# Optimization experiments

Hardware: AMD Instinct MI355X
Metric: run time of the kernel (lower is better)

## Reference

```python
import jax, jax.numpy as jnp
import numpy as np

HIDDEN = 1024
HEADS = 16
HEAD_DIM = HIDDEN // HEADS


def setup_inputs() -> dict:
    key = jax.random.key(0)
    ks = jax.random.split(key, 9)
    B, S, D = 8, 1370, HIDDEN
    x = jax.random.normal(ks[0], (B, S, D), dtype=jnp.float32)
    s = 1.0 / np.sqrt(D)
    Wq = jax.random.normal(ks[1], (D, D), dtype=jnp.float32) * s
    bq = jnp.zeros((D,), dtype=jnp.float32)
    Wk = jax.random.normal(ks[2], (D, D), dtype=jnp.float32) * s
    bk = jnp.zeros((D,), dtype=jnp.float32)
    Wv = jax.random.normal(ks[3], (D, D), dtype=jnp.float32) * s
    bv = jnp.zeros((D,), dtype=jnp.float32)
    Wo = jax.random.normal(ks[4], (D, D), dtype=jnp.float32) * s
    bo = jnp.zeros((D,), dtype=jnp.float32)
    return {"x": x, "Wq": Wq, "bq": bq, "Wk": Wk, "bk": bk,
            "Wv": Wv, "bv": bv, "Wo": Wo, "bo": bo}


def reference(x, Wq, bq, Wk, bk, Wv, bv, Wo, bo):
    B, S, D = x.shape
    H, Dh = HEADS, HEAD_DIM
    # separate Q/K/V projections
    q = (x @ Wq + bq).reshape(B, S, H, Dh).transpose(0, 2, 1, 3)  # [B,H,S,Dh]
    k = (x @ Wk + bk).reshape(B, S, H, Dh).transpose(0, 2, 1, 3)
    v = (x @ Wv + bv).reshape(B, S, H, Dh).transpose(0, 2, 1, 3)
    scale = jnp.asarray(Dh, q.dtype) ** -0.5
    attn = jnp.einsum('bhqd,bhkd->bhqk', q, k) * scale  # [B,H,S,S]
    attn = jax.nn.softmax(attn, axis=-1)
    out = jnp.einsum('bhqk,bhkd->bhqd', attn, v)        # [B,H,S,Dh]
    out = out.transpose(0, 2, 1, 3).reshape(B, S, D)
    return out @ Wo + bo
```

## Files before the change

kernel.cpp:

```cpp
#include <hip/hip_runtime.h>
#include <stdint.h>

#define DEV __device__ __forceinline__

typedef unsigned short u16;
typedef __attribute__((ext_vector_type(8))) __bf16 bf16x8;
typedef __attribute__((ext_vector_type(8))) u16 u16x8;
typedef __attribute__((ext_vector_type(4))) u16 u16x4;
typedef __attribute__((ext_vector_type(4))) float floatx4;

#define S_LEN 1370
#define S_PAD 1408
#define NH 16
#define DH 64
#define M_TOK (8 * S_LEN)
#define NKT (S_PAD / 64)
#define CEXP 0.18033688f

DEV u16 f2bf(float f) {
    union { float f; uint32_t u; } v; v.f = f;
    uint32_t u = v.u + 0x7fffu + ((v.u >> 16) & 1u);
    return (u16)(u >> 16);
}

typedef const __attribute__((address_space(1))) void as1_cvoid;
typedef __attribute__((address_space(3))) void as3_void;

DEV void async16(const void* g, void* s) {
    __builtin_amdgcn_global_load_lds((as1_cvoid*)g, (as3_void*)s, 16, 0, 0);
}

__global__ void cvt_bf16(const float* __restrict__ src, u16* __restrict__ dst) {
    const size_t i0 = ((size_t)blockIdx.x * 256 + threadIdx.x) * 8;
    const float4 a = *(const float4*)(src + i0);
    const float4 b = *(const float4*)(src + i0 + 4);
    u16x8 o;
    o[0] = f2bf(a.x); o[1] = f2bf(a.y); o[2] = f2bf(a.z); o[3] = f2bf(a.w);
    o[4] = f2bf(b.x); o[5] = f2bf(b.y); o[6] = f2bf(b.z); o[7] = f2bf(b.w);
    *(u16x8*)(dst + i0) = o;
}

__global__ void transpose4(const float* __restrict__ w0, const float* __restrict__ w1,
                           const float* __restrict__ w2, const float* __restrict__ w3,
                           u16* __restrict__ t0, u16* __restrict__ t1,
                           u16* __restrict__ t2, u16* __restrict__ t3) {
    __shared__ u16 tile[64][65];
    const float* src; u16* dst;
    switch (blockIdx.z) {
        case 0: src = w0; dst = t0; break;
        case 1: src = w1; dst = t1; break;
        case 2: src = w2; dst = t2; break;
        default: src = w3; dst = t3; break;
    }
    const int tx = blockIdx.x, ty = blockIdx.y, tid = threadIdx.x;
#pragma unroll
    for (int i = 0; i < 16; i++) {
        int e = i * 256 + tid, r = e >> 6, c = e & 63;
        tile[r][c] = f2bf(src[(size_t)(ty * 64 + r) * 1024 + tx * 64 + c]);
    }
    __syncthreads();
#pragma unroll
    for (int i = 0; i < 16; i++) {
        int e = i * 256 + tid, r = e >> 6, c = e & 63;
        dst[(size_t)(tx * 64 + r) * 1024 + ty * 64 + c] = tile[c][r];
    }
}

#define GEMM_KLOOP(M_, N_)                                                     \
    floatx4 acc[4][4];                                                         \
    _Pragma("unroll")                                                          \
    for (int i = 0; i < 4; i++)                                                \
        _Pragma("unroll")                                                      \
        for (int j = 0; j < 4; j++) acc[i][j] = (floatx4){0.f, 0.f, 0.f, 0.f}; \
    const int srow = tid >> 2;                                                 \
    const int kb = (tid & 3) * 16;                                             \
    int ar0 = mbase + srow;          if (ar0 > (M_) - 1) ar0 = (M_) - 1;       \
    int ar1 = mbase + 64 + srow;     if (ar1 > (M_) - 1) ar1 = (M_) - 1;       \
    int br0 = nbase + srow;          if (br0 > (N_) - 1) br0 = (N_) - 1;       \
    int br1 = nbase + 64 + srow;     if (br1 > (N_) - 1) br1 = (N_) - 1;       \
    const char* pA = (const char*)A;                                           \
    const char* pB = (const char*)BT;                                          \
    char* ldsA = (char*)As + w * 1024;                                         \
    char* ldsB = (char*)Bs + w * 1024;                                         \
    for (int kt = 0; kt < 32; kt++) {                                          \
        const int koff = kt * 64 + kb;                                         \
        async16(pA + (size_t)ar0 * 2048 + koff, ldsA);                         \
        async16(pA + (size_t)ar1 * 2048 + koff, ldsA + 4096);                  \
        async16(pB + (size_t)br0 * 2048 + koff, ldsB);                         \
        async16(pB + (size_t)br1 * 2048 + koff, ldsB + 4096);                  \
        __syncthreads();                                                       \
        bf16x8 af[4], bfv[4];                                                  \
        _Pragma("unroll")                                                      \
        for (int mi = 0; mi < 4; mi++)                                         \
            af[mi] = __builtin_bit_cast(bf16x8,                                \
                *(const u16x8*)&As[(wm + mi * 16 + l15) * 32 + quad * 8]);     \
        _Pragma("unroll")                                                      \
        for (int ni = 0; ni < 4; ni++)                                         \
            bfv[ni] = __builtin_bit_cast(bf16x8,                               \
                *(const u16x8*)&Bs[(wn + ni * 16 + l15) * 32 + quad * 8]);     \
        _Pragma("unroll")                                                      \
        for (int mi = 0; mi < 4; mi++)                                         \
            _Pragma("unroll")                                                  \
            for (int ni = 0; ni < 4; ni++)                                     \
                acc[mi][ni] = __builtin_amdgcn_mfma_f32_16x16x32_bf16(         \
                    af[mi], bfv[ni], acc[mi][ni], 0, 0, 0);                    \
        __syncthreads();                                                       \
    }

__global__ void gemm_qk(const u16* __restrict__ A, const u16* __restrict__ BT,
                        const float* __restrict__ bq, const float* __restrict__ bk,
                        u16* __restrict__ Cq, u16* __restrict__ Ck, int M) {
    __shared__ u16 As[128 * 32];
    __shared__ u16 Bs[128 * 32];
    const int tid = threadIdx.x;
    const int w = tid >> 6, lane = tid & 63, quad = lane >> 4, l15 = lane & 15;
    const int mbase = blockIdx.x * 128, nbase = blockIdx.y * 128;
    const int wm = (w >> 1) * 64, wn = (w & 1) * 64;

    GEMM_KLOOP(M, 2048)

    const bool isQ = nbase < 1024;
    u16* C = isQ ? Cq : Ck;
    const float* bias = isQ ? bq : bk;
    const float scale = isQ ? CEXP : 1.0f;
    const int nb = (isQ ? nbase : nbase - 1024) + wn;
#pragma unroll
    for (int ni = 0; ni < 4; ni++) {
        const int n = nb + ni * 16 + l15;
        const float bv = bias[n];
#pragma unroll
        for (int mi = 0; mi < 4; mi++)
#pragma unroll
            for (int r = 0; r < 4; r++) {
                const int m = mbase + wm + mi * 16 + quad * 4 + r;
                if (m < M) C[(size_t)m * 1024 + n] = f2bf((acc[mi][ni][r] + bv) * scale);
            }
    }
}

template <int MODE>
__global__ void gemm_bt(const u16* __restrict__ A, const u16* __restrict__ BT,
                        const float* __restrict__ bias, void* __restrict__ Cv,
                        int M, int N) {
    __shared__ u16 As[128 * 32];
    __shared__ u16 Bs[128 * 32];
    const int tid = threadIdx.x;
    const int w = tid >> 6, lane = tid & 63, quad = lane >> 4, l15 = lane & 15;
    const int mbase = blockIdx.x * 128, nbase = blockIdx.y * 128;
    const int wm = (w >> 1) * 64, wn = (w & 1) * 64;

    GEMM_KLOOP(M, N)

    if (MODE == 2) {
#pragma unroll
        for (int ni = 0; ni < 4; ni++) {
            const int n = nbase + wn + ni * 16 + l15;
            const float bv = bias[n];
#pragma unroll
            for (int mi = 0; mi < 4; mi++)
#pragma unroll
                for (int r = 0; r < 4; r++) {
                    const int m = mbase + wm + mi * 16 + quad * 4 + r;
                    if (m < M) ((float*)Cv)[(size_t)m * 1024 + n] = acc[mi][ni][r] + bv;
                }
        }
    } else {
        u16* C = (u16*)Cv;
#pragma unroll
        for (int mi = 0; mi < 4; mi++)
#pragma unroll
            for (int r = 0; r < 4; r++) {
                const int mf = mbase + wm + mi * 16 + quad * 4 + r;
                const int h = mf >> 6, d = mf & 63;
                const float bv = bias[mf];
#pragma unroll
                for (int ni = 0; ni < 4; ni++) {
                    const int t = nbase + wn + ni * 16 + l15;
                    if (t < N) {
                        const int b = t / S_LEN;
                        const int s = t - b * S_LEN;
                        C[(size_t)((b * NH + h) * DH + d) * S_PAD + s] =
                            f2bf(acc[mi][ni][r] + bv);
                    }
                }
            }
    }
}

__global__ void flash_attn(const u16* __restrict__ Q, const u16* __restrict__ K,
                           const u16* __restrict__ VT, u16* __restrict__ O) {
    __shared__ u16 Ks[2][2 * 64 * 32];
    __shared__ u16 Vs[2][2 * 64 * 32];
    __shared__ u16 Ps[4][32 * 72];

    const int tid = threadIdx.x;
    const int w = tid >> 6, lane = tid & 63, quad = lane >> 4, l15 = lane & 15;
    const int bh = blockIdx.x, b = bh >> 4, h = bh & 15;
    const int q0 = blockIdx.y * 128 + w * 32;

    bf16x8 qf[2][2];
#pragma unroll
    for (int mi = 0; mi < 2; mi++) {
        int qr = q0 + mi * 16 + l15;
        if (qr > S_LEN - 1) qr = S_LEN - 1;
        const u16* qp = Q + (size_t)(b * S_LEN + qr) * 1024 + h * 64 + quad * 8;
        qf[mi][0] = __builtin_bit_cast(bf16x8, *(const u16x8*)qp);
        qf[mi][1] = __builtin_bit_cast(bf16x8, *(const u16x8*)(qp + 32));
    }

    floatx4 o_acc[2][4];
#pragma unroll
    for (int mi = 0; mi < 2; mi++)
#pragma unroll
        for (int nd = 0; nd < 4; nd++) o_acc[mi][nd] = (floatx4){0.f, 0.f, 0.f, 0.f};
    float lacc[2] = {0.f, 0.f};

    const int lrow = lane >> 2;
    const int scol = ((lane & 3) ^ ((lane >> 3) & 3)) * 16;
    const char* Kbl = (const char*)K + ((size_t)b * S_LEN * 1024 + h * 64) * 2 + scol;
    const char* Vbl = (const char*)VT +
                      ((size_t)(bh * 64 + w * 16 + lrow) * S_PAD) * 2 + scol;
    char* KsB = (char*)Ks;
    char* VsB = (char*)Vs;
    u16* Pw = Ps[w];

    const int rcol = (quad ^ ((l15 >> 1) & 3)) * 16;

#define STAGE(KT, BI)                                                          \
    {                                                                          \
        int key_ = (KT) * 64 + w * 16 + lrow;                                  \
        if (key_ > S_LEN - 1) key_ = S_LEN - 1;                                \
        const char* kg_ = Kbl + (size_t)key_ * 2048;                           \
        char* kd_ = KsB + (BI) * 8192 + (w * 16) * 64;                         \
        async16(kg_, kd_);                                                     \
        async16(kg_ + 64, kd_ + 4096);                                         \
        const char* vg_ = Vbl + (KT) * 128;                                    \
        char* vd_ = VsB + (BI) * 8192 + (w * 16) * 64;                         \
        async16(vg_, vd_);                                                     \
        async16(vg_ + 64, vd_ + 4096);                                         \
    }

    STAGE(0, 0)
    __syncthreads();

    for (int kt = 0; kt < NKT; kt++) {
        const int bi = kt & 1;
        if (kt + 1 < NKT) STAGE(kt + 1, bi ^ 1)
        const char* KsT = KsB + bi * 8192;
        const char* VsT = VsB + bi * 8192;

        floatx4 st[2][4];
#pragma unroll
        for (int mi = 0; mi < 2; mi++)
#pragma unroll
            for (int ni = 0; ni < 4; ni++) st[mi][ni] = (floatx4){0.f, 0.f, 0.f, 0.f};
#pragma unroll
        for (int kk = 0; kk < 2; kk++)
#pragma unroll
            for (int ni = 0; ni < 4; ni++) {
                bf16x8 kf = __builtin_bit_cast(bf16x8,
                    *(const u16x8*)(KsT + kk * 4096 + (ni * 16 + l15) * 64 + rcol));
                st[0][ni] = __builtin_amdgcn_mfma_f32_16x16x32_bf16(kf, qf[0][kk], st[0][ni], 0, 0, 0);
                st[1][ni] = __builtin_amdgcn_mfma_f32_16x16x32_bf16(kf, qf[1][kk], st[1][ni], 0, 0, 0);
            }

        if (kt == NKT - 1) {
#pragma unroll
            for (int ni = 0; ni < 4; ni++)
#pragma unroll
                for (int r = 0; r < 4; r++) {
                    const bool oob = (kt * 64 + ni * 16 + quad * 4 + r) >= S_LEN;
                    if (oob) { st[0][ni][r] = -16384.f; st[1][ni][r] = -16384.f; }
                }
        }

#pragma unroll
        for (int mi = 0; mi < 2; mi++)
#pragma unroll
            for (int ni = 0; ni < 4; ni++) {
                u16x4 pq;
#pragma unroll
                for (int r = 0; r < 4; r++) {
                    const float p = __builtin_amdgcn_exp2f(st[mi][ni][r]);
                    lacc[mi] += p;
                    union { float f; uint32_t u; } cv; cv.f = p;
                    pq[r] = (u16)((cv.u + 0x8000u) >> 16);
                }
                *(u16x4*)&Pw[(mi * 16 + l15) * 72 + ni * 16 + quad * 4] = pq;
            }

        __asm__ __volatile__("" ::: "memory");

#pragma unroll
        for (int kk = 0; kk < 2; kk++) {
            bf16x8 pf0 = __builtin_bit_cast(bf16x8,
                *(const u16x8*)&Pw[(l15) * 72 + kk * 32 + quad * 8]);
            bf16x8 pf1 = __builtin_bit_cast(bf16x8,
                *(const u16x8*)&Pw[(16 + l15) * 72 + kk * 32 + quad * 8]);
#pragma unroll
            for (int nd = 0; nd < 4; nd++) {
                bf16x8 vf = __builtin_bit_cast(bf16x8,
                    *(const u16x8*)(VsT + kk * 4096 + (nd * 16 + l15) * 64 + rcol));
                o_acc[0][nd] = __builtin_amdgcn_mfma_f32_16x16x32_bf16(pf0, vf, o_acc[0][nd], 0, 0, 0);
                o_acc[1][nd] = __builtin_amdgcn_mfma_f32_16x16x32_bf16(pf1, vf, o_acc[1][nd], 0, 0, 0);
            }
        }
        __syncthreads();
    }

    float linv[2];
#pragma unroll
    for (int mi = 0; mi < 2; mi++) {
        float rs = lacc[mi];
        rs += __shfl_xor(rs, 16);
        rs += __shfl_xor(rs, 32);
        linv[mi] = 1.f / rs;
    }

#pragma unroll
    for (int mi = 0; mi < 2; mi++)
#pragma unroll
        for (int r = 0; r < 4; r++) {
            const float inv = __shfl(linv[mi], quad * 4 + r);
            const int q = q0 + mi * 16 + quad * 4 + r;
            if (q < S_LEN) {
                u16* op = O + (size_t)(b * S_LEN + q) * 1024 + h * 64;
#pragma unroll
                for (int nd = 0; nd < 4; nd++)
                    op[nd * 16 + l15] = f2bf(o_acc[mi][nd][r] * inv);
            }
        }
}

extern "C" void kernel_launch(void* const* d_in, const int* in_sizes, int n_in,
                              void* d_out, int out_size, void* d_ws, size_t ws_size,
                              hipStream_t stream) {
    const float* x  = (const float*)d_in[0];
    const float* Wq = (const float*)d_in[1];
    const float* bq = (const float*)d_in[2];
    const float* Wk = (const float*)d_in[3];
    const float* bk = (const float*)d_in[4];
    const float* Wv = (const float*)d_in[5];
    const float* bv = (const float*)d_in[6];
    const float* Wo = (const float*)d_in[7];
    const float* bo = (const float*)d_in[8];
    float* out = (float*)d_out;

    u16* WqT = (u16*)d_ws;
    u16* WkT = WqT + (size_t)1024 * 1024;
    u16* WvT = WkT + (size_t)1024 * 1024;
    u16* WoT = WvT + (size_t)1024 * 1024;
    u16* xb  = WoT + (size_t)1024 * 1024;
    u16* Qb  = xb + (size_t)M_TOK * 1024;
    u16* Kb  = Qb + (size_t)M_TOK * 1024;
    u16* VTb = Kb + (size_t)M_TOK * 1024;
    u16* Ob  = VTb + (size_t)128 * 64 * S_PAD;

    cvt_bf16<<<dim3(M_TOK * 1024 / 2048), 256, 0, stream>>>(x, xb);
    transpose4<<<dim3(16, 16, 4), 256, 0, stream>>>(Wq, Wk, Wv, Wo, WqT, WkT, WvT, WoT);
    gemm_qk<<<dim3(86, 16), 256, 0, stream>>>(xb, WqT, bq, bk, Qb, Kb, M_TOK);
    gemm_bt<1><<<dim3(8, 86), 256, 0, stream>>>(WvT, xb, bv, VTb, 1024, M_TOK);
    flash_attn<<<dim3(128, 11), 256, 0, stream>>>(Qb, Kb, VTb, Ob);
    gemm_bt<2><<<dim3(86, 8), 256, 0, stream>>>(Ob, WoT, bo, out, M_TOK, 1024);
}
```

Before: 369.6 us.

## Replace projection GEMMs with 256x256 double-buffered pipelined kernel, fuse QKV

Replaces the 128x128 synchronous-per-k-step GEMMs with a 512-thread 256x256 tile kernel. It double-buffers LDS, issues async global-to-LDS loads interleaved with the MFMA phases, uses XOR-swizzled LDS addressing, and adds explicit barriers and s_setprio. The V projection is folded into one QKV launch, with the V^T transposed layout written in the epilogue. The output projection uses the same core. This aims to hide memory latency and raise MFMA utilisation. In exchange it takes large LDS (~129KB) and register pressure, and the 256-wide tiles waste more work on the M padding.

New measurement: 406.8 us. +10.1%, slower.

```diff
diff --git a/kernel.cpp b/kernel.cpp
--- a/kernel.cpp
+++ b/kernel.cpp
@@ -66,125 +66,173 @@
     }
 }
 
-#define GEMM_KLOOP(M_, N_)                                                     \
-    floatx4 acc[4][4];                                                         \
-    _Pragma("unroll")                                                          \
-    for (int i = 0; i < 4; i++)                                                \
-        _Pragma("unroll")                                                      \
-        for (int j = 0; j < 4; j++) acc[i][j] = (floatx4){0.f, 0.f, 0.f, 0.f}; \
-    const int srow = tid >> 2;                                                 \
-    const int kb = (tid & 3) * 16;                                             \
-    int ar0 = mbase + srow;          if (ar0 > (M_) - 1) ar0 = (M_) - 1;       \
-    int ar1 = mbase + 64 + srow;     if (ar1 > (M_) - 1) ar1 = (M_) - 1;       \
-    int br0 = nbase + srow;          if (br0 > (N_) - 1) br0 = (N_) - 1;       \
-    int br1 = nbase + 64 + srow;     if (br1 > (N_) - 1) br1 = (N_) - 1;       \
-    const char* pA = (const char*)A;                                           \
-    const char* pB = (const char*)BT;                                          \
-    char* ldsA = (char*)As + w * 1024;                                         \
-    char* ldsB = (char*)Bs + w * 1024;                                         \
-    for (int kt = 0; kt < 32; kt++) {                                          \
-        const int koff = kt * 64 + kb;                                         \
-        async16(pA + (size_t)ar0 * 2048 + koff, ldsA);                         \
-        async16(pA + (size_t)ar1 * 2048 + koff, ldsA + 4096);                  \
-        async16(pB + (size_t)br0 * 2048 + koff, ldsB);                         \
-        async16(pB + (size_t)br1 * 2048 + koff, ldsB + 4096);                  \
-        __syncthreads();                                                       \
-        bf16x8 af[4], bfv[4];                                                  \
-        _Pragma("unroll")                                                      \
-        for (int mi = 0; mi < 4; mi++)                                         \
-            af[mi] = __builtin_bit_cast(bf16x8,                                \
-                *(const u16x8*)&As[(wm + mi * 16 + l15) * 32 + quad * 8]);     \
-        _Pragma("unroll")                                                      \
-        for (int ni = 0; ni < 4; ni++)                                         \
-            bfv[ni] = __builtin_bit_cast(bf16x8,                               \
-                *(const u16x8*)&Bs[(wn + ni * 16 + l15) * 32 + quad * 8]);     \
-        _Pragma("unroll")                                                      \
-        for (int mi = 0; mi < 4; mi++)                                         \
-            _Pragma("unroll")                                                  \
-            for (int ni = 0; ni < 4; ni++)                                     \
-                acc[mi][ni] = __builtin_amdgcn_mfma_f32_16x16x32_bf16(         \
-                    af[mi], bfv[ni], acc[mi][ni], 0, 0, 0);                    \
-        __syncthreads();                                                       \
-    }
-
-__global__ void gemm_qk(const u16* __restrict__ A, const u16* __restrict__ BT,
-                        const float* __restrict__ bq, const float* __restrict__ bk,
-                        u16* __restrict__ Cq, u16* __restrict__ Ck, int M) {
-    __shared__ u16 As[128 * 32];
-    __shared__ u16 Bs[128 * 32];
-    const int tid = threadIdx.x;
-    const int w = tid >> 6, lane = tid & 63, quad = lane >> 4, l15 = lane & 15;
-    const int mbase = blockIdx.x * 128, nbase = blockIdx.y * 128;
-    const int wm = (w >> 1) * 64, wn = (w & 1) * 64;
-
-    GEMM_KLOOP(M, 2048)
-
-    const bool isQ = nbase < 1024;
-    u16* C = isQ ? Cq : Ck;
-    const float* bias = isQ ? bq : bk;
-    const float scale = isQ ? CEXP : 1.0f;
-    const int nb = (isQ ? nbase : nbase - 1024) + wn;
-#pragma unroll
-    for (int ni = 0; ni < 4; ni++) {
-        const int n = nb + ni * 16 + l15;
-        const float bv = bias[n];
-#pragma unroll
-        for (int mi = 0; mi < 4; mi++)
-#pragma unroll
-            for (int r = 0; r < 4; r++) {
-                const int m = mbase + wm + mi * 16 + quad * 4 + r;
-                if (m < M) C[(size_t)m * 1024 + n] = f2bf((acc[mi][ni][r] + bv) * scale);
-            }
-    }
-}
-
-template <int MODE>
-__global__ void gemm_bt(const u16* __restrict__ A, const u16* __restrict__ BT,
-                        const float* __restrict__ bias, void* __restrict__ Cv,
-                        int M, int N) {
-    __shared__ u16 As[128 * 32];
-    __shared__ u16 Bs[128 * 32];
-    const int tid = threadIdx.x;
-    const int w = tid >> 6, lane = tid & 63, quad = lane >> 4, l15 = lane & 15;
-    const int mbase = blockIdx.x * 128, nbase = blockIdx.y * 128;
-    const int wm = (w >> 1) * 64, wn = (w & 1) * 64;
-
-    GEMM_KLOOP(M, N)
-
-    if (MODE == 2) {
-#pragma unroll
-        for (int ni = 0; ni < 4; ni++) {
-            const int n = nbase + wn + ni * 16 + l15;
-            const float bv = bias[n];
-#pragma unroll
-            for (int mi = 0; mi < 4; mi++)
-#pragma unroll
-                for (int r = 0; r < 4; r++) {
-                    const int m = mbase + wm + mi * 16 + quad * 4 + r;
-                    if (m < M) ((float*)Cv)[(size_t)m * 1024 + n] = acc[mi][ni][r] + bv;
-                }
-        }
+#define GNT   16
+#define GHALF 16384
+#define GBOFF 32768
+#define GBUFB 65536
+#define GSCR  131072
+#define GSMEM 132096
+
+#define GSRC(P, R, RM) \
+    ((const char*)(P) + (size_t)((R) < (RM) ? (R) : (RM) - 1) * 2048 + clog)
+
+#define GSTAGE(SRCP, LOFF, TK) { \
+    const int tk_ = (TK) < GNT ? (TK) : GNT - 1; \
+    const int l0_ = (TK) < GNT ? (LOFF) + (w * 2) * 1024 : GSCR; \
+    const int l1_ = (TK) < GNT ? (LOFF) + (w * 2 + 1) * 1024 : GSCR; \
+    async16(SRCP[0] + tk_ * 128, smem + l0_); \
+    async16(SRCP[1] + tk_ * 128, smem + l1_); }
+
+#define GLOADA(OFF) \
+    _Pragma("unroll") for (int mi = 0; mi < 4; mi++) { \
+        afr[mi][0] = __builtin_bit_cast(bf16x8, \
+            *(const u16x8*)(smem + (OFF) + rowA + mi * 2048 + csw0)); \
+        afr[mi][1] = __builtin_bit_cast(bf16x8, \
+            *(const u16x8*)(smem + (OFF) + rowA + mi * 2048 + csw1)); }
+
+#define GLOADB(DST, OFF) \
+    _Pragma("unroll") for (int ni = 0; ni < 2; ni++) { \
+        DST[ni][0] = __builtin_bit_cast(bf16x8, \
+            *(const u16x8*)(smem + (OFF) + rowB + ni * 2048 + csw0)); \
+        DST[ni][1] = __builtin_bit_cast(bf16x8, \
+            *(const u16x8*)(smem + (OFF) + rowB + ni * 2048 + csw1)); }
+
+#define GMID \
+    __builtin_amdgcn_sched_barrier(0); \
+    __builtin_amdgcn_s_barrier(); \
+    __builtin_amdgcn_sched_barrier(0); \
+    __builtin_amdgcn_s_setprio(1);
+
+#define GEND \
+    __builtin_amdgcn_s_setprio(0); \
+    __builtin_amdgcn_sched_barrier(0); \
+    __builtin_amdgcn_s_barrier(); \
+    __builtin_amdgcn_sched_barrier(0);
+
+#define GENDV \
+    __builtin_amdgcn_s_setprio(0); \
+    asm volatile("s_waitcnt vmcnt(4)" ::: "memory"); \
+    __builtin_amdgcn_sched_barrier(0); \
+    __builtin_amdgcn_s_barrier(); \
+    __builtin_amdgcn_sched_barrier(0);
+
+#define GMFMA(MH, NH_, BR) \
+    _Pragma("unroll") for (int kk = 0; kk < 2; kk++) \
+    _Pragma("unroll") for (int mi = 0; mi < 4; mi++) \
+    _Pragma("unroll") for (int ni = 0; ni < 2; ni++) \
+        acc[MH][NH_][mi][ni] = __builtin_amdgcn_mfma_f32_16x16x32_bf16( \
+            afr[mi][kk], BR[ni][kk], acc[MH][NH_][mi][ni], 0, 0, 0);
+
+#define GEMM256_CORE(M_, N_) \
+    __shared__ alignas(16) char smem[GSMEM]; \
+    const int tid = threadIdx.x; \
+    const int w = tid >> 6, lane = tid & 63; \
+    const int quad = lane >> 4, l15 = lane & 15; \
+    const int wr = w >> 2, wc = w & 3; \
+    const int mbase = blockIdx.x * 256, nbase = blockIdx.y * 256; \
+    const int rh0 = w * 16 + (lane >> 3), rh1 = rh0 + 8; \
+    const int clog = ((lane & 7) ^ (lane >> 3)) * 16;         \
+    const char* sA0[2] = {GSRC(A, mbase + rh0, M_), GSRC(A, mbase + rh1, M_)}; \
+    const char* sA1[2] = {GSRC(A, mbase + 128 + rh0, M_), GSRC(A, mbase + 128 + rh1, M_)}; \
+    const char* sB0[2] = {GSRC(BT, nbase + rh0, N_), GSRC(BT, nbase + rh1, N_)}; \
+    const char* sB1[2] = {GSRC(BT, nbase + 128 + rh0, N_), GSRC(BT, nbase + 128 + rh1, N_)}; \
+    const int rowA = (wr * 64 + l15) * 128, rowB = (wc * 32 + l15) * 128; \
+    const int csw0 = (quad ^ (l15 & 7)) * 16;                 \
+    const int csw1 = ((4 + quad) ^ (l15 & 7)) * 16; \
+    floatx4 acc[2][2][4][2]; \
+    _Pragma("unroll") for (int a_ = 0; a_ < 2; a_++) \
+    _Pragma("unroll") for (int b_ = 0; b_ < 2; b_++) \
+    _Pragma("unroll") for (int c_ = 0; c_ < 4; c_++) \
+    _Pragma("unroll") for (int d_ = 0; d_ < 2; d_++) \
+        acc[a_][b_][c_][d_] = (floatx4){0.f, 0.f, 0.f, 0.f}; \
+     \
+    GSTAGE(sA0, 0, 0) \
+    GSTAGE(sB0, GBOFF, 0) \
+    GSTAGE(sB1, GBOFF + GHALF, 0) \
+    GSTAGE(sA1, GHALF, 0) \
+    GSTAGE(sA0, GBUFB, 1) \
+    GSTAGE(sB0, GBUFB + GBOFF, 1) \
+    asm volatile("s_waitcnt vmcnt(4)" ::: "memory"); \
+    __builtin_amdgcn_s_barrier(); \
+    __builtin_amdgcn_sched_barrier(0); \
+    bf16x8 afr[4][2], b0r[2][2], b1r[2][2]; \
+    _Pragma("unroll 1") for (int it = 0; it < 8; it++) { \
+        const int t1 = 2 * it + 1, t2 = 2 * it + 2, t3 = 2 * it + 3; \
+         \
+        GLOADA(0) GLOADB(b0r, GBOFF) \
+        GSTAGE(sB1, GBUFB + GBOFF + GHALF, t1) \
+        GMID GMFMA(0, 0, b0r) GEND \
+         \
+        GLOADB(b1r, GBOFF + GHALF) \
+        GSTAGE(sA1, GBUFB + GHALF, t1) \
+        GMID GMFMA(0, 1, b1r) GEND \
+         \
+        GLOADA(GHALF) \
+        GSTAGE(sA0, 0, t2) \
+        GMID GMFMA(1, 0, b0r) GEND \
+         \
+        GSTAGE(sB0, GBOFF, t2) \
+        GMID GMFMA(1, 1, b1r) GENDV \
+         \
+        GLOADA(GBUFB) GLOADB(b0r, GBUFB + GBOFF) \
+        GSTAGE(sB1, GBOFF + GHALF, t2) \
+        GMID GMFMA(0, 0, b0r) GEND \
+         \
+        GLOADB(b1r, GBUFB + GBOFF + GHALF) \
+        GSTAGE(sA1, GHALF, t2) \
+        GMID GMFMA(0, 1, b1r) GEND \
+         \
+        GLOADA(GBUFB + GHALF) \
+        GSTAGE(sA0, GBUFB, t3) \
+        GMID GMFMA(1, 0, b0r) GEND \
+         \
+        GSTAGE(sB0, GBUFB + GBOFF, t3) \
+        GMID GMFMA(1, 1, b1r) GENDV \
+    } \
+    asm volatile("s_waitcnt vmcnt(0)" ::: "memory");
+
+#define GEPILOGUE(...) \
+    _Pragma("unroll") for (int mh = 0; mh < 2; mh++) \
+    _Pragma("unroll") for (int nh = 0; nh < 2; nh++) \
+    _Pragma("unroll") for (int mi = 0; mi < 4; mi++) \
+    _Pragma("unroll") for (int ni = 0; ni < 2; ni++) \
+    _Pragma("unroll") for (int r = 0; r < 4; r++) { \
+        const int row = mbase + mh * 128 + wr * 64 + mi * 16 + quad * 4 + r; \
+        const int col = nbase + nh * 128 + wc * 32 + ni * 16 + l15; \
+        const float av = acc[mh][nh][mi][ni][r]; \
+        __VA_ARGS__ }
+
+__global__ __launch_bounds__(512, 2) void gemm_qkv256(
+        const u16* __restrict__ A, const u16* __restrict__ BT,
+        const float* __restrict__ bq, const float* __restrict__ bk,
+        const float* __restrict__ bv, u16* __restrict__ Cq,
+        u16* __restrict__ Ck, u16* __restrict__ VT, int M) {
+    GEMM256_CORE(M, 3072)
+    const int sel = nbase >> 10;
+    if (sel == 0) {
+        GEPILOGUE(
+            if (row < M) Cq[(size_t)row * 1024 + col] = f2bf((av + bq[col]) * CEXP);)
+    } else if (sel == 1) {
+        GEPILOGUE(
+            const int n2 = col - 1024;
+            if (row < M) Ck[(size_t)row * 1024 + n2] = f2bf(av + bk[n2]);)
     } else {
-        u16* C = (u16*)Cv;
-#pragma unroll
-        for (int mi = 0; mi < 4; mi++)
-#pragma unroll
-            for (int r = 0; r < 4; r++) {
-                const int mf = mbase + wm + mi * 16 + quad * 4 + r;
-                const int h = mf >> 6, d = mf & 63;
-                const float bv = bias[mf];
-#pragma unroll
-                for (int ni = 0; ni < 4; ni++) {
-                    const int t = nbase + wn + ni * 16 + l15;
-                    if (t < N) {
-                        const int b = t / S_LEN;
-                        const int s = t - b * S_LEN;
-                        C[(size_t)((b * NH + h) * DH + d) * S_PAD + s] =
-                            f2bf(acc[mi][ni][r] + bv);
-                    }
-                }
-            }
-    }
+        GEPILOGUE(
+            const int fe = col - 2048;
+            if (row < M) {
+                const int bb = row / S_LEN;
+                const int ss = row - bb * S_LEN;
+                VT[(size_t)((bb * NH + (fe >> 6)) * DH + (fe & 63)) * S_PAD + ss] =
+                    f2bf(av + bv[fe]);
+            })
+    }
+}
+
+__global__ __launch_bounds__(512, 2) void gemm_o256(
+        const u16* __restrict__ A, const u16* __restrict__ BT,
+        const float* __restrict__ bias, float* __restrict__ C, int M) {
+    GEMM256_CORE(M, 1024)
+    GEPILOGUE(if (row < M) C[(size_t)row * 1024 + col] = av + bias[col];)
 }
 
 __global__ void flash_attn(const u16* __restrict__ Q, const u16* __restrict__ K,
@@ -358,8 +406,7 @@
 
     cvt_bf16<<<dim3(M_TOK * 1024 / 2048), 256, 0, stream>>>(x, xb);
     transpose4<<<dim3(16, 16, 4), 256, 0, stream>>>(Wq, Wk, Wv, Wo, WqT, WkT, WvT, WoT);
-    gemm_qk<<<dim3(86, 16), 256, 0, stream>>>(xb, WqT, bq, bk, Qb, Kb, M_TOK);
-    gemm_bt<1><<<dim3(8, 86), 256, 0, stream>>>(WvT, xb, bv, VTb, 1024, M_TOK);
+    gemm_qkv256<<<dim3(43, 12), 512, 0, stream>>>(xb, WqT, bq, bk, bv, Qb, Kb, VTb, M_TOK);
     flash_attn<<<dim3(128, 11), 256, 0, stream>>>(Qb, Kb, VTb, Ob);
-    gemm_bt<2><<<dim3(86, 8), 256, 0, stream>>>(Ob, WoT, bo, out, M_TOK, 1024);
-}
+    gemm_o256<<<dim3(43, 4), 512, 0, stream>>>(Ob, WoT, bo, out, M_TOK);
+}
```

## Fuse QKV projections into one GEMM and single-buffer attention K/V staging

Applied to the files above, without the earlier changes.

Merges the separate Q/K projection and transposed V projection kernels into one GEMM over 3072 output columns, with the V tile written directly into the transposed per-head layout. The output projection gets its own specialized kernel. Flash attention drops double-buffered K/V shared memory in favour of a single buffer that is loaded, waited on and synchronized each iteration. This reduces launches and shared memory, but loses the overlap of global loads with compute, and the V epilogue now uses strided scattered stores.

After: 364.5 us. About the same (-1.4%).

```diff
diff --git a/kernel.cpp b/kernel.cpp
--- a/kernel.cpp
+++ b/kernel.cpp
@@ -107,9 +107,10 @@
         __syncthreads();                                                       \
     }
 
-__global__ void gemm_qk(const u16* __restrict__ A, const u16* __restrict__ BT,
-                        const float* __restrict__ bq, const float* __restrict__ bk,
-                        u16* __restrict__ Cq, u16* __restrict__ Ck, int M) {
+__global__ void gemm_qkv(const u16* __restrict__ A, const u16* __restrict__ BT,
+                         const float* __restrict__ bq, const float* __restrict__ bk,
+                         const float* __restrict__ bv, u16* __restrict__ Cq,
+                         u16* __restrict__ Ck, u16* __restrict__ VT, int M) {
     __shared__ u16 As[128 * 32];
     __shared__ u16 Bs[128 * 32];
     const int tid = threadIdx.x;
@@ -117,31 +118,59 @@
     const int mbase = blockIdx.x * 128, nbase = blockIdx.y * 128;
     const int wm = (w >> 1) * 64, wn = (w & 1) * 64;
 
-    GEMM_KLOOP(M, 2048)
-
-    const bool isQ = nbase < 1024;
-    u16* C = isQ ? Cq : Ck;
-    const float* bias = isQ ? bq : bk;
-    const float scale = isQ ? CEXP : 1.0f;
-    const int nb = (isQ ? nbase : nbase - 1024) + wn;
-#pragma unroll
-    for (int ni = 0; ni < 4; ni++) {
-        const int n = nb + ni * 16 + l15;
-        const float bv = bias[n];
-#pragma unroll
-        for (int mi = 0; mi < 4; mi++)
-#pragma unroll
-            for (int r = 0; r < 4; r++) {
-                const int m = mbase + wm + mi * 16 + quad * 4 + r;
-                if (m < M) C[(size_t)m * 1024 + n] = f2bf((acc[mi][ni][r] + bv) * scale);
-            }
-    }
-}
-
-template <int MODE>
-__global__ void gemm_bt(const u16* __restrict__ A, const u16* __restrict__ BT,
-                        const float* __restrict__ bias, void* __restrict__ Cv,
-                        int M, int N) {
+    GEMM_KLOOP(M, 3072)
+
+    const int sel = nbase >> 10;
+    if (sel == 0) {
+#pragma unroll
+        for (int ni = 0; ni < 4; ni++) {
+            const int n = nbase + wn + ni * 16 + l15;
+            const float bb = bq[n];
+#pragma unroll
+            for (int mi = 0; mi < 4; mi++)
+#pragma unroll
+                for (int r = 0; r < 4; r++) {
+                    const int m = mbase + wm + mi * 16 + quad * 4 + r;
+                    if (m < M) Cq[(size_t)m * 1024 + n] = f2bf((acc[mi][ni][r] + bb) * CEXP);
+                }
+        }
+    } else if (sel == 1) {
+#pragma unroll
+        for (int ni = 0; ni < 4; ni++) {
+            const int n = nbase - 1024 + wn + ni * 16 + l15;
+            const float bb = bk[n];
+#pragma unroll
+            for (int mi = 0; mi < 4; mi++)
+#pragma unroll
+                for (int r = 0; r < 4; r++) {
+                    const int m = mbase + wm + mi * 16 + quad * 4 + r;
+                    if (m < M) Ck[(size_t)m * 1024 + n] = f2bf(acc[mi][ni][r] + bb);
+                }
+        }
+    } else {
+#pragma unroll
+        for (int ni = 0; ni < 4; ni++) {
+            const int fe = nbase - 2048 + wn + ni * 16 + l15;
+            const float bb = bv[fe];
+            const int hh = fe >> 6, dd = fe & 63;
+#pragma unroll
+            for (int mi = 0; mi < 4; mi++)
+#pragma unroll
+                for (int r = 0; r < 4; r++) {
+                    const int m = mbase + wm + mi * 16 + quad * 4 + r;
+                    if (m < M) {
+                        const int btk = m / S_LEN;
+                        const int ss = m - btk * S_LEN;
+                        VT[(size_t)((btk * NH + hh) * DH + dd) * S_PAD + ss] =
+                            f2bf(acc[mi][ni][r] + bb);
+                    }
+                }
+        }
+    }
+}
+
+__global__ void gemm_o(const u16* __restrict__ A, const u16* __restrict__ BT,
+                       const float* __restrict__ bias, float* __restrict__ C, int M) {
     __shared__ u16 As[128 * 32];
     __shared__ u16 Bs[128 * 32];
     const int tid = threadIdx.x;
@@ -149,48 +178,26 @@
     const int mbase = blockIdx.x * 128, nbase = blockIdx.y * 128;
     const int wm = (w >> 1) * 64, wn = (w & 1) * 64;
 
-    GEMM_KLOOP(M, N)
-
-    if (MODE == 2) {
-#pragma unroll
-        for (int ni = 0; ni < 4; ni++) {
-            const int n = nbase + wn + ni * 16 + l15;
-            const float bv = bias[n];
-#pragma unroll
-            for (int mi = 0; mi < 4; mi++)
-#pragma unroll
-                for (int r = 0; r < 4; r++) {
-                    const int m = mbase + wm + mi * 16 + quad * 4 + r;
-                    if (m < M) ((float*)Cv)[(size_t)m * 1024 + n] = acc[mi][ni][r] + bv;
-                }
-        }
-    } else {
-        u16* C = (u16*)Cv;
+    GEMM_KLOOP(M, 1024)
+
+#pragma unroll
+    for (int ni = 0; ni < 4; ni++) {
+        const int n = nbase + wn + ni * 16 + l15;
+        const float bb = bias[n];
 #pragma unroll
         for (int mi = 0; mi < 4; mi++)
 #pragma unroll
             for (int r = 0; r < 4; r++) {
-                const int mf = mbase + wm + mi * 16 + quad * 4 + r;
-                const int h = mf >> 6, d = mf & 63;
-                const float bv = bias[mf];
-#pragma unroll
-                for (int ni = 0; ni < 4; ni++) {
-                    const int t = nbase + wn + ni * 16 + l15;
-                    if (t < N) {
-                        const int b = t / S_LEN;
-                        const int s = t - b * S_LEN;
-                        C[(size_t)((b * NH + h) * DH + d) * S_PAD + s] =
-                            f2bf(acc[mi][ni][r] + bv);
-                    }
-                }
+                const int m = mbase + wm + mi * 16 + quad * 4 + r;
+                if (m < M) C[(size_t)m * 1024 + n] = acc[mi][ni][r] + bb;
             }
     }
 }
 
 __global__ void flash_attn(const u16* __restrict__ Q, const u16* __restrict__ K,
                            const u16* __restrict__ VT, u16* __restrict__ O) {
-    __shared__ u16 Ks[2][2 * 64 * 32];
-    __shared__ u16 Vs[2][2 * 64 * 32];
+    __shared__ u16 Ks[2 * 64 * 32];
+    __shared__ u16 Vs[2 * 64 * 32];
     __shared__ u16 Ps[4][32 * 72];
 
     const int tid = threadIdx.x;
@@ -226,29 +233,25 @@
 
     const int rcol = (quad ^ ((l15 >> 1) & 3)) * 16;
 
-#define STAGE(KT, BI)                                                          \
+#define STAGE(KT)                                                              \
     {                                                                          \
         int key_ = (KT) * 64 + w * 16 + lrow;                                  \
         if (key_ > S_LEN - 1) key_ = S_LEN - 1;                                \
         const char* kg_ = Kbl + (size_t)key_ * 2048;                           \
-        char* kd_ = KsB + (BI) * 8192 + (w * 16) * 64;                         \
+        char* kd_ = KsB + (w * 16) * 64;                                       \
         async16(kg_, kd_);                                                     \
         async16(kg_ + 64, kd_ + 4096);                                         \
         const char* vg_ = Vbl + (KT) * 128;                                    \
-        char* vd_ = VsB + (BI) * 8192 + (w * 16) * 64;                         \
+        char* vd_ = VsB + (w * 16) * 64;                                       \
         async16(vg_, vd_);                                                     \
         async16(vg_ + 64, vd_ + 4096);                                         \
     }
 
-    STAGE(0, 0)
+    STAGE(0)
+    asm volatile("s_waitcnt vmcnt(0)" ::: "memory");
     __syncthreads();
 
     for (int kt = 0; kt < NKT; kt++) {
-        const int bi = kt & 1;
-        if (kt + 1 < NKT) STAGE(kt + 1, bi ^ 1)
-        const char* KsT = KsB + bi * 8192;
-        const char* VsT = VsB + bi * 8192;
-
         floatx4 st[2][4];
 #pragma unroll
         for (int mi = 0; mi < 2; mi++)
@@ -259,7 +262,7 @@
 #pragma unroll
             for (int ni = 0; ni < 4; ni++) {
                 bf16x8 kf = __builtin_bit_cast(bf16x8,
-                    *(const u16x8*)(KsT + kk * 4096 + (ni * 16 + l15) * 64 + rcol));
+                    *(const u16x8*)(KsB + kk * 4096 + (ni * 16 + l15) * 64 + rcol));
                 st[0][ni] = __builtin_amdgcn_mfma_f32_16x16x32_bf16(kf, qf[0][kk], st[0][ni], 0, 0, 0);
                 st[1][ni] = __builtin_amdgcn_mfma_f32_16x16x32_bf16(kf, qf[1][kk], st[1][ni], 0, 0, 0);
             }
@@ -300,12 +303,18 @@
 #pragma unroll
             for (int nd = 0; nd < 4; nd++) {
                 bf16x8 vf = __builtin_bit_cast(bf16x8,
-                    *(const u16x8*)(VsT + kk * 4096 + (nd * 16 + l15) * 64 + rcol));
+                    *(const u16x8*)(VsB + kk * 4096 + (nd * 16 + l15) * 64 + rcol));
                 o_acc[0][nd] = __builtin_amdgcn_mfma_f32_16x16x32_bf16(pf0, vf, o_acc[0][nd], 0, 0, 0);
                 o_acc[1][nd] = __builtin_amdgcn_mfma_f32_16x16x32_bf16(pf1, vf, o_acc[1][nd], 0, 0, 0);
             }
         }
+
         __syncthreads();
+        if (kt + 1 < NKT) {
+            STAGE(kt + 1)
+            asm volatile("s_waitcnt vmcnt(0)" ::: "memory");
+            __syncthreads();
+        }
     }
 
     float linv[2];
@@ -358,8 +367,7 @@
 
     cvt_bf16<<<dim3(M_TOK * 1024 / 2048), 256, 0, stream>>>(x, xb);
     transpose4<<<dim3(16, 16, 4), 256, 0, stream>>>(Wq, Wk, Wv, Wo, WqT, WkT, WvT, WoT);
-    gemm_qk<<<dim3(86, 16), 256, 0, stream>>>(xb, WqT, bq, bk, Qb, Kb, M_TOK);
-    gemm_bt<1><<<dim3(8, 86), 256, 0, stream>>>(WvT, xb, bv, VTb, 1024, M_TOK);
+    gemm_qkv<<<dim3(86, 24), 256, 0, stream>>>(xb, WqT, bq, bk, bv, Qb, Kb, VTb, M_TOK);
     flash_attn<<<dim3(128, 11), 256, 0, stream>>>(Qb, Kb, VTb, Ob);
-    gemm_bt<2><<<dim3(86, 8), 256, 0, stream>>>(Ob, WoT, bo, out, M_TOK, 1024);
-}
+    gemm_o<<<dim3(86, 8), 256, 0, stream>>>(Ob, WoT, bo, out, M_TOK);
+}
```
